# Kernel optimization log

Hardware: AMD Instinct MI355X
Metric: run time of the kernel (lower is better)

## Reference

```python
import jax, jax.numpy as jnp
import numpy as np

B, S, D, H = 4, 2048, 1024, 16
DK = D // H  # 64


def setup_inputs() -> dict:
    key = jax.random.key(0)
    ks = jax.random.split(key, 9)
    x = jax.random.normal(ks[0], (B, S, D), dtype=jnp.float32)
    # causal mask, broadcast over batch and heads
    attn_mask = jnp.tril(jnp.ones((S, S), dtype=jnp.int32))[None, None]
    scale = 0.02
    Wq = jax.random.normal(ks[1], (D, D), dtype=jnp.float32) * scale
    Wk = jax.random.normal(ks[2], (D, D), dtype=jnp.float32) * scale
    Wv = jax.random.normal(ks[3], (D, D), dtype=jnp.float32) * scale
    Wo = jax.random.normal(ks[4], (D, D), dtype=jnp.float32) * scale
    bq = jax.random.normal(ks[5], (D,), dtype=jnp.float32) * scale
    bk = jax.random.normal(ks[6], (D,), dtype=jnp.float32) * scale
    bv = jax.random.normal(ks[7], (D,), dtype=jnp.float32) * scale
    bo = jax.random.normal(ks[8], (D,), dtype=jnp.float32) * scale
    return {"x": x, "attn_mask": attn_mask, "Wq": Wq, "bq": bq, "Wk": Wk,
            "bk": bk, "Wv": Wv, "bv": bv, "Wo": Wo, "bo": bo}


def reference(x, attn_mask, Wq, bq, Wk, bk, Wv, bv, Wo, bo):
    b, s, d = x.shape
    # projections -> [b, h, s, dk]
    def proj(W, bias):
        return (x @ W + bias).reshape(b, s, H, DK).transpose(0, 2, 1, 3)
    q = proj(Wq, bq)
    k = proj(Wk, bk)
    v = proj(Wv, bv)
    # scores [b, h, s, s]
    scores = jnp.einsum('bhqd,bhkd->bhqk', q, k) / jnp.sqrt(jnp.float32(DK))
    scores = jnp.where(attn_mask == 0, jnp.float32(-1e9), scores)
    probs = jax.nn.softmax(scores, axis=-1)  # dropout_rate=0 -> identity
    attn_out = jnp.einsum('bhqk,bhkd->bhqd', probs, v)
    # combine heads -> [b, s, d], then output projection
    attn_out = attn_out.transpose(0, 2, 1, 3).reshape(b, s, d)
    return attn_out @ Wo + bo
```

## Files before the change

kernel.cpp:

```cpp
#include <hip/hip_runtime.h>
#include <hip/hip_bf16.h>
#include <stdint.h>

#define S_LEN 2048
#define DMODEL 1024
#define NH 16
#define DK 64
#define BATCH 4
#define KDIM 1024
#define SCQ 0.18033688f

using bf16 = __hip_bfloat16;
using bf162 = __hip_bfloat162;

typedef __bf16 v_bf16x8 __attribute__((ext_vector_type(8)));
typedef short v_s16x4 __attribute__((ext_vector_type(4)));
typedef float v_f32x4 __attribute__((ext_vector_type(4)));

union PackB4 { v_s16x4 v; bf162 h[2]; };

struct alignas(8) BF4 { bf16 a, b, c, d; };

__global__ __launch_bounds__(256) void cvt_f32_bf16(const float* __restrict__ in,
                                                    bf16* __restrict__ out) {
    size_t i = ((size_t)blockIdx.x * 256 + threadIdx.x) * 4;
    float4 v = *(const float4*)(in + i);
    BF4 r;
    r.a = __float2bfloat16(v.x);
    r.b = __float2bfloat16(v.y);
    r.c = __float2bfloat16(v.z);
    r.d = __float2bfloat16(v.w);
    *(BF4*)(out + i) = r;
}

__global__ __launch_bounds__(256) void transpose_cvt4(
    const float* __restrict__ W0, const float* __restrict__ W1,
    const float* __restrict__ W2, const float* __restrict__ W3,
    bf16* __restrict__ Wt4) {
    __shared__ float tile[32][33];
    const int z = blockIdx.z;
    const float* W = (z == 0) ? W0 : (z == 1) ? W1 : (z == 2) ? W2 : W3;
    bf16* Wt = Wt4 + (size_t)z * DMODEL * DMODEL;
    const float sc = (z == 0) ? SCQ : 1.0f;
    int tx = threadIdx.x, ty = threadIdx.y;
    int k0 = blockIdx.x * 32, n0 = blockIdx.y * 32;
    #pragma unroll
    for (int i = 0; i < 4; i++) {
        int k = k0 + ty + 8 * i;
        tile[ty + 8 * i][tx] = W[(size_t)k * DMODEL + n0 + tx];
    }
    __syncthreads();
    #pragma unroll
    for (int i = 0; i < 4; i++) {
        int n = n0 + ty + 8 * i;
        Wt[(size_t)n * DMODEL + k0 + tx] = __float2bfloat16(tile[tx][ty + 8 * i] * sc);
    }
}

__global__ __launch_bounds__(256) void gemm_qkv(
    const bf16* __restrict__ A, const bf16* __restrict__ Wt4,
    const float* __restrict__ bq, const float* __restrict__ bk,
    const float* __restrict__ bv,
    bf16* __restrict__ Qo, bf16* __restrict__ Ko, bf16* __restrict__ Vto)
{
    __shared__ __align__(16) short As[128 * 32];
    __shared__ __align__(16) short Bs[128 * 32];
    const int z = blockIdx.z;
    const bf16* Bt = Wt4 + (size_t)z * DMODEL * DMODEL;
    const float* bias = (z == 0) ? bq : (z == 1) ? bk : bv;
    const float bsc = (z == 0) ? SCQ : 1.0f;

    const int t = threadIdx.x;
    const int lane = t & 63;
    const int wave = t >> 6;
    const int quad = lane >> 4;
    const int l15 = lane & 15;
    const int m0 = blockIdx.x * 128;
    const int n0 = blockIdx.y * 128;
    const int wRow = (wave >> 1) * 64;
    const int wCol = (wave & 1) * 64;

    const int r0 = t >> 2, p0 = t & 3;
    const int r1 = (t + 256) >> 2, p1 = (t + 256) & 3;

    const short* ArowBase = (z == 2) ? Bs : As;
    const short* BrowBase = (z == 2) ? As : Bs;

    v_f32x4 acc[4][4] = {};

    for (int k0 = 0; k0 < KDIM; k0 += 32) {
        uint4 a0 = *(const uint4*)(A + (size_t)(m0 + r0) * KDIM + k0 + p0 * 8);
        uint4 a1 = *(const uint4*)(A + (size_t)(m0 + r1) * KDIM + k0 + p1 * 8);
        uint4 b0 = *(const uint4*)(Bt + (size_t)(n0 + r0) * KDIM + k0 + p0 * 8);
        uint4 b1 = *(const uint4*)(Bt + (size_t)(n0 + r1) * KDIM + k0 + p1 * 8);
        __syncthreads();
        *(uint4*)(As + r0 * 32 + p0 * 8) = a0;
        *(uint4*)(As + r1 * 32 + p1 * 8) = a1;
        *(uint4*)(Bs + r0 * 32 + p0 * 8) = b0;
        *(uint4*)(Bs + r1 * 32 + p1 * 8) = b1;
        __syncthreads();

        v_bf16x8 af[4], bfr[4];
        #pragma unroll
        for (int mt = 0; mt < 4; mt++) {
            int r = wRow + mt * 16 + l15;
            af[mt] = *(const v_bf16x8*)(ArowBase + r * 32 + quad * 8);
        }
        #pragma unroll
        for (int nt = 0; nt < 4; nt++) {
            int r = wCol + nt * 16 + l15;
            bfr[nt] = *(const v_bf16x8*)(BrowBase + r * 32 + quad * 8);
        }
        #pragma unroll
        for (int mt = 0; mt < 4; mt++)
            #pragma unroll
            for (int nt = 0; nt < 4; nt++)
                acc[mt][nt] = __builtin_amdgcn_mfma_f32_16x16x32_bf16(
                    af[mt], bfr[nt], acc[mt][nt], 0, 0, 0);
    }

    if (z != 2) {
        bf16* C = (z == 0) ? Qo : Ko;
        float bvv[4];
        #pragma unroll
        for (int nt = 0; nt < 4; nt++)
            bvv[nt] = bias[n0 + wCol + nt * 16 + l15] * bsc;
        #pragma unroll
        for (int mt = 0; mt < 4; mt++)
            #pragma unroll
            for (int nt = 0; nt < 4; nt++)
                #pragma unroll
                for (int r = 0; r < 4; r++) {
                    int row = m0 + wRow + mt * 16 + quad * 4 + r;
                    int col = n0 + wCol + nt * 16 + l15;
                    int b = row >> 11, s = row & (S_LEN - 1);
                    int h = col >> 6, dk = col & (DK - 1);
                    C[(((size_t)(b * NH + h)) * S_LEN + s) * DK + dk] =
                        __float2bfloat16(acc[mt][nt][r] + bvv[nt]);
                }
    } else {
        float bvv[4][4];
        #pragma unroll
        for (int mt = 0; mt < 4; mt++)
            #pragma unroll
            for (int r = 0; r < 4; r++)
                bvv[mt][r] = bias[n0 + wRow + mt * 16 + quad * 4 + r];
        #pragma unroll
        for (int mt = 0; mt < 4; mt++)
            #pragma unroll
            for (int nt = 0; nt < 4; nt++)
                #pragma unroll
                for (int r = 0; r < 4; r++) {
                    int ng = n0 + wRow + mt * 16 + quad * 4 + r;
                    int rowg = m0 + wCol + nt * 16 + l15;
                    int b = rowg >> 11, s = rowg & (S_LEN - 1);
                    int h = ng >> 6, dk = ng & (DK - 1);
                    Vto[(((size_t)(b * NH + h)) * DK + dk) * S_LEN + s] =
                        __float2bfloat16(acc[mt][nt][r] + bvv[mt][r]);
                }
    }
}

__global__ __launch_bounds__(256) void gemm_o(
    const bf16* __restrict__ A, const bf16* __restrict__ Bt,
    const float* __restrict__ bias, float* __restrict__ C)
{
    __shared__ __align__(16) short As[128 * 32];
    __shared__ __align__(16) short Bs[128 * 32];
    const int t = threadIdx.x;
    const int lane = t & 63;
    const int wave = t >> 6;
    const int quad = lane >> 4;
    const int l15 = lane & 15;
    const int m0 = blockIdx.x * 128;
    const int n0 = blockIdx.y * 128;
    const int wRow = (wave >> 1) * 64;
    const int wCol = (wave & 1) * 64;

    const int r0 = t >> 2, p0 = t & 3;
    const int r1 = (t + 256) >> 2, p1 = (t + 256) & 3;

    v_f32x4 acc[4][4] = {};

    for (int k0 = 0; k0 < KDIM; k0 += 32) {
        uint4 a0 = *(const uint4*)(A + (size_t)(m0 + r0) * KDIM + k0 + p0 * 8);
        uint4 a1 = *(const uint4*)(A + (size_t)(m0 + r1) * KDIM + k0 + p1 * 8);
        uint4 b0 = *(const uint4*)(Bt + (size_t)(n0 + r0) * KDIM + k0 + p0 * 8);
        uint4 b1 = *(const uint4*)(Bt + (size_t)(n0 + r1) * KDIM + k0 + p1 * 8);
        __syncthreads();
        *(uint4*)(As + r0 * 32 + p0 * 8) = a0;
        *(uint4*)(As + r1 * 32 + p1 * 8) = a1;
        *(uint4*)(Bs + r0 * 32 + p0 * 8) = b0;
        *(uint4*)(Bs + r1 * 32 + p1 * 8) = b1;
        __syncthreads();

        v_bf16x8 af[4], bfr[4];
        #pragma unroll
        for (int mt = 0; mt < 4; mt++) {
            int r = wRow + mt * 16 + l15;
            af[mt] = *(const v_bf16x8*)(As + r * 32 + quad * 8);
        }
        #pragma unroll
        for (int nt = 0; nt < 4; nt++) {
            int r = wCol + nt * 16 + l15;
            bfr[nt] = *(const v_bf16x8*)(Bs + r * 32 + quad * 8);
        }
        #pragma unroll
        for (int mt = 0; mt < 4; mt++)
            #pragma unroll
            for (int nt = 0; nt < 4; nt++)
                acc[mt][nt] = __builtin_amdgcn_mfma_f32_16x16x32_bf16(
                    af[mt], bfr[nt], acc[mt][nt], 0, 0, 0);
    }

    float bvv[4];
    #pragma unroll
    for (int nt = 0; nt < 4; nt++) bvv[nt] = bias[n0 + wCol + nt * 16 + l15];

    #pragma unroll
    for (int mt = 0; mt < 4; mt++)
        #pragma unroll
        for (int nt = 0; nt < 4; nt++)
            #pragma unroll
            for (int r = 0; r < 4; r++) {
                int row = m0 + wRow + mt * 16 + quad * 4 + r;
                int col = n0 + wCol + nt * 16 + l15;
                C[(size_t)row * DMODEL + col] = acc[mt][nt][r] + bvv[nt];
            }
}

__global__ __launch_bounds__(256) void attn_mfma(
    const bf16* __restrict__ Qg, const bf16* __restrict__ Kg,
    const bf16* __restrict__ Vtg, bf16* __restrict__ Og)
{
    __shared__ __align__(16) short lds[16896];
    short* Ks = lds;
    short* Vs = lds + 8192;

    const int t = threadIdx.x;
    const int lane = t & 63;
    const int wave = t >> 6;
    const int quad = lane >> 4;
    const int l15 = lane & 15;
    const int bh = blockIdx.x;
    const int yy = (gridDim.y - 1) - blockIdx.y;
    const int q0 = yy * 128;

    const size_t baseK = (size_t)bh * S_LEN * DK;
    const size_t baseVt = (size_t)bh * DK * S_LEN;

    v_bf16x8 qf[2][2];
    #pragma unroll
    for (int qt = 0; qt < 2; qt++) {
        int q = q0 + wave * 32 + qt * 16 + l15;
        #pragma unroll
        for (int kc = 0; kc < 2; kc++)
            qf[qt][kc] = *(const v_bf16x8*)(Qg + baseK + (size_t)q * DK + kc * 32 + quad * 8);
    }

    v_f32x4 oacc[2][4] = {};
    float mrun[2] = {-1e30f, -1e30f};
    float lrun[2] = {0.f, 0.f};

    for (int tt = 0; tt <= yy; tt++) {
        int k0 = tt * 128;
        __syncthreads();
        #pragma unroll
        for (int i = 0; i < 4; i++) {
            int c = t + 256 * i;
            int r = c >> 3, p = c & 7;
            uint4 val = *(const uint4*)(Kg + baseK + (size_t)(k0 + r) * DK + p * 8);
            *(uint4*)(Ks + r * 64 + (p ^ (r & 7)) * 8) = val;
        }
        #pragma unroll
        for (int i = 0; i < 4; i++) {
            int c = t + 256 * i;
            int d = c >> 4, p = c & 15;
            uint4 val = *(const uint4*)(Vtg + baseVt + (size_t)d * S_LEN + k0 + p * 8);
            *(uint4*)(Vs + d * 136 + p * 8) = val;
        }
        __syncthreads();

        v_f32x4 s_[8][2];
        #pragma unroll
        for (int kt = 0; kt < 8; kt++) {
            int krow = kt * 16 + l15;
            v_bf16x8 kf0 = *(const v_bf16x8*)(Ks + krow * 64 + ((quad) ^ (krow & 7)) * 8);
            v_bf16x8 kf1 = *(const v_bf16x8*)(Ks + krow * 64 + ((4 + quad) ^ (krow & 7)) * 8);
            #pragma unroll
            for (int qt = 0; qt < 2; qt++) {
                v_f32x4 a = {};
                a = __builtin_amdgcn_mfma_f32_16x16x32_bf16(kf0, qf[qt][0], a, 0, 0, 0);
                a = __builtin_amdgcn_mfma_f32_16x16x32_bf16(kf1, qf[qt][1], a, 0, 0, 0);
                s_[kt][qt] = a;
            }
        }

        if (tt == yy) {
            #pragma unroll
            for (int kt = 0; kt < 8; kt++)
                #pragma unroll
                for (int qt = 0; qt < 2; qt++) {
                    int qq = wave * 32 + qt * 16 + l15;
                    #pragma unroll
                    for (int r = 0; r < 4; r++) {
                        int key = kt * 16 + quad * 4 + r;
                        if (key > qq) s_[kt][qt][r] = -1e30f;
                    }
                }
        }

        float tmax[2] = {-1e30f, -1e30f};
        #pragma unroll
        for (int kt = 0; kt < 8; kt++)
            #pragma unroll
            for (int qt = 0; qt < 2; qt++)
                #pragma unroll
                for (int r = 0; r < 4; r++)
                    tmax[qt] = fmaxf(tmax[qt], s_[kt][qt][r]);
        #pragma unroll
        for (int qt = 0; qt < 2; qt++) {
            tmax[qt] = fmaxf(tmax[qt], __shfl_xor(tmax[qt], 16));
            tmax[qt] = fmaxf(tmax[qt], __shfl_xor(tmax[qt], 32));
        }
        float alpha[2];
        #pragma unroll
        for (int qt = 0; qt < 2; qt++) {
            float mn = fmaxf(mrun[qt], tmax[qt]);
            alpha[qt] = __builtin_amdgcn_exp2f(mrun[qt] - mn);
            mrun[qt] = mn;
        }
        float lsum[2] = {0.f, 0.f};
        #pragma unroll
        for (int kt = 0; kt < 8; kt++)
            #pragma unroll
            for (int qt = 0; qt < 2; qt++)
                #pragma unroll
                for (int r = 0; r < 4; r++) {
                    float p = __builtin_amdgcn_exp2f(s_[kt][qt][r] - mrun[qt]);
                    s_[kt][qt][r] = p;
                    lsum[qt] += p;
                }
        #pragma unroll
        for (int qt = 0; qt < 2; qt++) {
            lsum[qt] += __shfl_xor(lsum[qt], 16);
            lsum[qt] += __shfl_xor(lsum[qt], 32);
            lrun[qt] = lrun[qt] * alpha[qt] + lsum[qt];
        }
        #pragma unroll
        for (int qt = 0; qt < 2; qt++)
            #pragma unroll
            for (int dt = 0; dt < 4; dt++)
                #pragma unroll
                for (int r = 0; r < 4; r++)
                    oacc[qt][dt][r] *= alpha[qt];

        #pragma unroll
        for (int kt = 0; kt < 8; kt++) {
            v_s16x4 vf[4];
            #pragma unroll
            for (int dt = 0; dt < 4; dt++)
                vf[dt] = *(const v_s16x4*)(Vs + (dt * 16 + l15) * 136 + kt * 16 + quad * 4);
            #pragma unroll
            for (int qt = 0; qt < 2; qt++) {
                PackB4 pu;
                pu.h[0] = __float22bfloat162_rn(make_float2(s_[kt][qt][0], s_[kt][qt][1]));
                pu.h[1] = __float22bfloat162_rn(make_float2(s_[kt][qt][2], s_[kt][qt][3]));
                #pragma unroll
                for (int dt = 0; dt < 4; dt++)
                    oacc[qt][dt] = __builtin_amdgcn_mfma_f32_16x16x16bf16_1k(
                        vf[dt], pu.v, oacc[qt][dt], 0, 0, 0);
            }
        }
    }

    __syncthreads();
    #pragma unroll
    for (int qt = 0; qt < 2; qt++) {
        float inv = 1.f / lrun[qt];
        int qloc = wave * 32 + qt * 16 + l15;
        #pragma unroll
        for (int dt = 0; dt < 4; dt++) {
            PackB4 ou;
            ou.h[0] = __float22bfloat162_rn(
                make_float2(oacc[qt][dt][0] * inv, oacc[qt][dt][1] * inv));
            ou.h[1] = __float22bfloat162_rn(
                make_float2(oacc[qt][dt][2] * inv, oacc[qt][dt][3] * inv));
            *(v_s16x4*)(lds + qloc * 72 + dt * 16 + quad * 4) = ou.v;
        }
    }
    __syncthreads();
    {
        const int b = bh >> 4, h = bh & 15;
        int row = t >> 1, half = t & 1;
        size_t gbase = (((size_t)b * S_LEN + q0 + row) * NH + h) * DK + half * 32;
        #pragma unroll
        for (int j = 0; j < 4; j++)
            *(uint4*)(Og + gbase + j * 8) =
                *(const uint4*)(lds + row * 72 + half * 32 + j * 8);
    }
}

extern "C" void kernel_launch(void* const* d_in, const int* in_sizes, int n_in,
                              void* d_out, int out_size, void* d_ws, size_t ws_size,
                              hipStream_t stream) {
    const float* x  = (const float*)d_in[0];
    const float* Wq = (const float*)d_in[2];
    const float* bq = (const float*)d_in[3];
    const float* Wk = (const float*)d_in[4];
    const float* bk = (const float*)d_in[5];
    const float* Wv = (const float*)d_in[6];
    const float* bv = (const float*)d_in[7];
    const float* Wo = (const float*)d_in[8];
    const float* bo = (const float*)d_in[9];
    float* out = (float*)d_out;

    const size_t TEN = (size_t)BATCH * S_LEN * DMODEL * sizeof(bf16);
    char* ws = (char*)d_ws;
    bf16* xb  = (bf16*)ws;
    bf16* Vt  = (bf16*)(ws + TEN);
    bf16* Wt4 = (bf16*)(ws + 2 * TEN);
    bf16* Q   = (bf16*)d_out;
    bf16* Kt  = (bf16*)((char*)d_out + TEN);
    bf16* AO  = xb;

    hipLaunchKernelGGL(cvt_f32_bf16, dim3(BATCH * S_LEN * DMODEL / 1024), dim3(256),
                       0, stream, x, xb);

    hipLaunchKernelGGL(transpose_cvt4, dim3(DMODEL / 32, DMODEL / 32, 4), dim3(32, 8),
                       0, stream, Wq, Wk, Wv, Wo, Wt4);

    hipLaunchKernelGGL(gemm_qkv, dim3(BATCH * S_LEN / 128, DMODEL / 128, 3), dim3(256),
                       0, stream, xb, Wt4, bq, bk, bv, Q, Kt, Vt);

    hipLaunchKernelGGL(attn_mfma, dim3(BATCH * NH, S_LEN / 128), dim3(256),
                       0, stream, Q, Kt, Vt, AO);

    hipLaunchKernelGGL(gemm_o, dim3(BATCH * S_LEN / 128, DMODEL / 128), dim3(256),
                       0, stream, AO, Wt4 + (size_t)3 * DMODEL * DMODEL, bo, out);
}
```

Before: 304.4 us.

## Fuse input fp32-to-bf16 conversion into projection GEMMs and swizzle V LDS tile

Drops the standalone x conversion kernel. Each projection GEMM now loads fp32 x directly and packs it to bf16 while filling shared memory. The single batched QKV launch is split into three templated launches, and the weight transposes and workspace layout are rearranged so Wo is converted after attention. The padded V tile in attention is replaced by an XOR-swizzled layout to save LDS while avoiding bank conflicts. The trade-off is that x is now read in fp32 three times, which is more global traffic than reading bf16 once, and the GEMMs lose cross-z concurrency.

```diff
diff --git a/kernel.cpp b/kernel.cpp
--- a/kernel.cpp
+++ b/kernel.cpp
@@ -18,30 +18,23 @@
 typedef float v_f32x4 __attribute__((ext_vector_type(4)));
 
 union PackB4 { v_s16x4 v; bf162 h[2]; };
-
-struct alignas(8) BF4 { bf16 a, b, c, d; };
-
-__global__ __launch_bounds__(256) void cvt_f32_bf16(const float* __restrict__ in,
-                                                    bf16* __restrict__ out) {
-    size_t i = ((size_t)blockIdx.x * 256 + threadIdx.x) * 4;
-    float4 v = *(const float4*)(in + i);
-    BF4 r;
-    r.a = __float2bfloat16(v.x);
-    r.b = __float2bfloat16(v.y);
-    r.c = __float2bfloat16(v.z);
-    r.d = __float2bfloat16(v.w);
-    *(BF4*)(out + i) = r;
-}
-
-__global__ __launch_bounds__(256) void transpose_cvt4(
-    const float* __restrict__ W0, const float* __restrict__ W1,
-    const float* __restrict__ W2, const float* __restrict__ W3,
-    bf16* __restrict__ Wt4) {
+struct alignas(16) S16x8 { v_s16x4 lo, hi; };
+
+__device__ __forceinline__ S16x8 pack8(const float* src) {
+    float4 f0 = *(const float4*)src;
+    float4 f1 = *(const float4*)(src + 4);
+    PackB4 a, b;
+    a.h[0] = __float22bfloat162_rn(make_float2(f0.x, f0.y));
+    a.h[1] = __float22bfloat162_rn(make_float2(f0.z, f0.w));
+    b.h[0] = __float22bfloat162_rn(make_float2(f1.x, f1.y));
+    b.h[1] = __float22bfloat162_rn(make_float2(f1.z, f1.w));
+    S16x8 r; r.lo = a.v; r.hi = b.v;
+    return r;
+}
+
+__global__ __launch_bounds__(256) void transpose_cvt(const float* __restrict__ W,
+                                                     bf16* __restrict__ Wt, float sc) {
     __shared__ float tile[32][33];
-    const int z = blockIdx.z;
-    const float* W = (z == 0) ? W0 : (z == 1) ? W1 : (z == 2) ? W2 : W3;
-    bf16* Wt = Wt4 + (size_t)z * DMODEL * DMODEL;
-    const float sc = (z == 0) ? SCQ : 1.0f;
     int tx = threadIdx.x, ty = threadIdx.y;
     int k0 = blockIdx.x * 32, n0 = blockIdx.y * 32;
     #pragma unroll
@@ -57,19 +50,13 @@
     }
 }
 
-__global__ __launch_bounds__(256) void gemm_qkv(
-    const bf16* __restrict__ A, const bf16* __restrict__ Wt4,
-    const float* __restrict__ bq, const float* __restrict__ bk,
-    const float* __restrict__ bv,
-    bf16* __restrict__ Qo, bf16* __restrict__ Ko, bf16* __restrict__ Vto)
+template <int MODE>
+__global__ __launch_bounds__(256) void gemm_projF(
+    const float* __restrict__ X, const bf16* __restrict__ Bt,
+    const float* __restrict__ bias, float bscale, bf16* __restrict__ C)
 {
     __shared__ __align__(16) short As[128 * 32];
     __shared__ __align__(16) short Bs[128 * 32];
-    const int z = blockIdx.z;
-    const bf16* Bt = Wt4 + (size_t)z * DMODEL * DMODEL;
-    const float* bias = (z == 0) ? bq : (z == 1) ? bk : bv;
-    const float bsc = (z == 0) ? SCQ : 1.0f;
-
     const int t = threadIdx.x;
     const int lane = t & 63;
     const int wave = t >> 6;
@@ -83,19 +70,16 @@
     const int r0 = t >> 2, p0 = t & 3;
     const int r1 = (t + 256) >> 2, p1 = (t + 256) & 3;
 
-    const short* ArowBase = (z == 2) ? Bs : As;
-    const short* BrowBase = (z == 2) ? As : Bs;
-
     v_f32x4 acc[4][4] = {};
 
     for (int k0 = 0; k0 < KDIM; k0 += 32) {
-        uint4 a0 = *(const uint4*)(A + (size_t)(m0 + r0) * KDIM + k0 + p0 * 8);
-        uint4 a1 = *(const uint4*)(A + (size_t)(m0 + r1) * KDIM + k0 + p1 * 8);
+        S16x8 a0 = pack8(X + (size_t)(m0 + r0) * KDIM + k0 + p0 * 8);
+        S16x8 a1 = pack8(X + (size_t)(m0 + r1) * KDIM + k0 + p1 * 8);
         uint4 b0 = *(const uint4*)(Bt + (size_t)(n0 + r0) * KDIM + k0 + p0 * 8);
         uint4 b1 = *(const uint4*)(Bt + (size_t)(n0 + r1) * KDIM + k0 + p1 * 8);
         __syncthreads();
-        *(uint4*)(As + r0 * 32 + p0 * 8) = a0;
-        *(uint4*)(As + r1 * 32 + p1 * 8) = a1;
+        *(S16x8*)(As + r0 * 32 + p0 * 8) = a0;
+        *(S16x8*)(As + r1 * 32 + p1 * 8) = a1;
         *(uint4*)(Bs + r0 * 32 + p0 * 8) = b0;
         *(uint4*)(Bs + r1 * 32 + p1 * 8) = b1;
         __syncthreads();
@@ -104,12 +88,12 @@
         #pragma unroll
         for (int mt = 0; mt < 4; mt++) {
             int r = wRow + mt * 16 + l15;
-            af[mt] = *(const v_bf16x8*)(ArowBase + r * 32 + quad * 8);
+            af[mt] = *(const v_bf16x8*)((MODE == 2 ? Bs : As) + r * 32 + quad * 8);
         }
         #pragma unroll
         for (int nt = 0; nt < 4; nt++) {
             int r = wCol + nt * 16 + l15;
-            bfr[nt] = *(const v_bf16x8*)(BrowBase + r * 32 + quad * 8);
+            bfr[nt] = *(const v_bf16x8*)((MODE == 2 ? As : Bs) + r * 32 + quad * 8);
         }
         #pragma unroll
         for (int mt = 0; mt < 4; mt++)
@@ -119,12 +103,11 @@
                     af[mt], bfr[nt], acc[mt][nt], 0, 0, 0);
     }
 
-    if (z != 2) {
-        bf16* C = (z == 0) ? Qo : Ko;
+    if (MODE == 1) {
         float bvv[4];
         #pragma unroll
         for (int nt = 0; nt < 4; nt++)
-            bvv[nt] = bias[n0 + wCol + nt * 16 + l15] * bsc;
+            bvv[nt] = bias[n0 + wCol + nt * 16 + l15] * bscale;
         #pragma unroll
         for (int mt = 0; mt < 4; mt++)
             #pragma unroll
@@ -155,7 +138,7 @@
                     int rowg = m0 + wCol + nt * 16 + l15;
                     int b = rowg >> 11, s = rowg & (S_LEN - 1);
                     int h = ng >> 6, dk = ng & (DK - 1);
-                    Vto[(((size_t)(b * NH + h)) * DK + dk) * S_LEN + s] =
+                    C[(((size_t)(b * NH + h)) * DK + dk) * S_LEN + s] =
                         __float2bfloat16(acc[mt][nt][r] + bvv[mt][r]);
                 }
     }
@@ -233,7 +216,7 @@
     const bf16* __restrict__ Qg, const bf16* __restrict__ Kg,
     const bf16* __restrict__ Vtg, bf16* __restrict__ Og)
 {
-    __shared__ __align__(16) short lds[16896];
+    __shared__ __align__(16) short lds[16384];
     short* Ks = lds;
     short* Vs = lds + 8192;
 
@@ -277,7 +260,7 @@
             int c = t + 256 * i;
             int d = c >> 4, p = c & 15;
             uint4 val = *(const uint4*)(Vtg + baseVt + (size_t)d * S_LEN + k0 + p * 8);
-            *(uint4*)(Vs + d * 136 + p * 8) = val;
+            *(uint4*)(Vs + d * 128 + ((p ^ (d & 15)) << 3)) = val;
         }
         __syncthreads();
 
@@ -359,8 +342,11 @@
         for (int kt = 0; kt < 8; kt++) {
             v_s16x4 vf[4];
             #pragma unroll
-            for (int dt = 0; dt < 4; dt++)
-                vf[dt] = *(const v_s16x4*)(Vs + (dt * 16 + l15) * 136 + kt * 16 + quad * 4);
+            for (int dt = 0; dt < 4; dt++) {
+                int d = dt * 16 + l15;
+                int ch = (2 * kt + (quad >> 1)) ^ (d & 15);
+                vf[dt] = *(const v_s16x4*)(Vs + d * 128 + (ch << 3) + (quad & 1) * 4);
+            }
             #pragma unroll
             for (int qt = 0; qt < 2; qt++) {
                 PackB4 pu;
@@ -416,26 +402,31 @@
     float* out = (float*)d_out;
 
     const size_t TEN = (size_t)BATCH * S_LEN * DMODEL * sizeof(bf16);
+    const size_t WSZ = (size_t)DMODEL * DMODEL * sizeof(bf16);
     char* ws = (char*)d_ws;
-    bf16* xb  = (bf16*)ws;
-    bf16* Vt  = (bf16*)(ws + TEN);
-    bf16* Wt4 = (bf16*)(ws + 2 * TEN);
-    bf16* Q   = (bf16*)d_out;
-    bf16* Kt  = (bf16*)((char*)d_out + TEN);
-    bf16* AO  = xb;
-
-    hipLaunchKernelGGL(cvt_f32_bf16, dim3(BATCH * S_LEN * DMODEL / 1024), dim3(256),
-                       0, stream, x, xb);
-
-    hipLaunchKernelGGL(transpose_cvt4, dim3(DMODEL / 32, DMODEL / 32, 4), dim3(32, 8),
-                       0, stream, Wq, Wk, Wv, Wo, Wt4);
-
-    hipLaunchKernelGGL(gemm_qkv, dim3(BATCH * S_LEN / 128, DMODEL / 128, 3), dim3(256),
-                       0, stream, xb, Wt4, bq, bk, bv, Q, Kt, Vt);
+    bf16* Q   = (bf16*)ws;
+    bf16* Kt  = (bf16*)(ws + TEN);
+    bf16* Vt  = (bf16*)(ws + 2 * TEN);
+    bf16* WtO = (bf16*)(ws + 2 * TEN);
+    bf16* WtQ = (bf16*)(ws + 3 * TEN);
+    bf16* WtK = (bf16*)(ws + 3 * TEN + WSZ);
+    bf16* WtV = (bf16*)(ws + 3 * TEN + 2 * WSZ);
+    bf16* AO  = (bf16*)(ws + 3 * TEN);
+
+    dim3 gT(DMODEL / 32, DMODEL / 32), bT(32, 8);
+    dim3 gG(BATCH * S_LEN / 128, DMODEL / 128);
+
+    hipLaunchKernelGGL(transpose_cvt, gT, bT, 0, stream, Wq, WtQ, SCQ);
+    hipLaunchKernelGGL(transpose_cvt, gT, bT, 0, stream, Wk, WtK, 1.0f);
+    hipLaunchKernelGGL(transpose_cvt, gT, bT, 0, stream, Wv, WtV, 1.0f);
+
+    hipLaunchKernelGGL((gemm_projF<1>), gG, dim3(256), 0, stream, x, WtQ, bq, SCQ, Q);
+    hipLaunchKernelGGL((gemm_projF<1>), gG, dim3(256), 0, stream, x, WtK, bk, 1.0f, Kt);
+    hipLaunchKernelGGL((gemm_projF<2>), gG, dim3(256), 0, stream, x, WtV, bv, 1.0f, Vt);
 
     hipLaunchKernelGGL(attn_mfma, dim3(BATCH * NH, S_LEN / 128), dim3(256),
                        0, stream, Q, Kt, Vt, AO);
 
-    hipLaunchKernelGGL(gemm_o, dim3(BATCH * S_LEN / 128, DMODEL / 128), dim3(256),
-                       0, stream, AO, Wt4 + (size_t)3 * DMODEL * DMODEL, bo, out);
-}
+    hipLaunchKernelGGL(transpose_cvt, gT, bT, 0, stream, Wo, WtO, 1.0f);
+    hipLaunchKernelGGL(gemm_o, gG, dim3(256), 0, stream, AO, WtO, bo, out);
+}
```

Result: slower. 339.2 us (+11.4%).
